# Performance work log

Measured on AMD Instinct MI355X. Metric: run time of the kernel, lower is better.

## Reference

```python
import jax, jax.numpy as jnp
import numpy as np

N, E = 50000, 800000
DIN, DH, DOUT = 128, 128, 64


def setup_inputs() -> dict:
    key = jax.random.key(0)
    ks = jax.random.split(key, 18)
    s = 0.05
    inp = {
        "x": jax.random.normal(ks[0], (N, DIN), dtype=jnp.float32),
        "edge_index": jax.random.randint(ks[1], (2, E), 0, N, dtype=jnp.int64),
        # conv1 MLP: Linear(DIN,DH), Linear(DH,DH)
        "c1_w1": jax.random.normal(ks[2], (DIN, DH), dtype=jnp.float32) * s,
        "c1_b1": jax.random.normal(ks[3], (DH,), dtype=jnp.float32) * s,
        "c1_w2": jax.random.normal(ks[4], (DH, DH), dtype=jnp.float32) * s,
        "c1_b2": jax.random.normal(ks[5], (DH,), dtype=jnp.float32) * s,
        # conv2 MLP
        "c2_w1": jax.random.normal(ks[6], (DH, DH), dtype=jnp.float32) * s,
        "c2_b1": jax.random.normal(ks[7], (DH,), dtype=jnp.float32) * s,
        "c2_w2": jax.random.normal(ks[8], (DH, DH), dtype=jnp.float32) * s,
        "c2_b2": jax.random.normal(ks[9], (DH,), dtype=jnp.float32) * s,
        # conv3 MLP
        "c3_w1": jax.random.normal(ks[10], (DH, DH), dtype=jnp.float32) * s,
        "c3_b1": jax.random.normal(ks[11], (DH,), dtype=jnp.float32) * s,
        "c3_w2": jax.random.normal(ks[12], (DH, DH), dtype=jnp.float32) * s,
        "c3_b2": jax.random.normal(ks[13], (DH,), dtype=jnp.float32) * s,
        # output head
        "lin1_w": jax.random.normal(ks[14], (DH, DH), dtype=jnp.float32) * s,
        "lin1_b": jax.random.normal(ks[15], (DH,), dtype=jnp.float32) * s,
        "lin2_w": jax.random.normal(ks[16], (DH, DOUT), dtype=jnp.float32) * s,
        "lin2_b": jax.random.normal(ks[17], (DOUT,), dtype=jnp.float32) * s,
    }
    return inp


def _gin_conv(h, src, dst, w1, b1, w2, b2):
    # PyG GINConv, eps=0: MLP((1+eps)*x + sum_{j->i} x_j)
    agg = jax.ops.segment_sum(h[src], dst, num_segments=h.shape[0])  # [N, D]
    z = h + agg
    z = jax.nn.relu(z @ w1 + b1)
    return jax.nn.relu(z @ w2 + b2)


def reference(x, edge_index, c1_w1, c1_b1, c1_w2, c1_b2,
              c2_w1, c2_b1, c2_w2, c2_b2,
              c3_w1, c3_b1, c3_w2, c3_b2,
              lin1_w, lin1_b, lin2_w, lin2_b):
    src, dst = edge_index[0], edge_index[1]
    h = _gin_conv(x, src, dst, c1_w1, c1_b1, c1_w2, c1_b2)
    h = jax.nn.relu(h)  # redundant after MLP ReLU, but faithful to source
    h = _gin_conv(h, src, dst, c2_w1, c2_b1, c2_w2, c2_b2)
    h = jax.nn.relu(h)
    h = _gin_conv(h, src, dst, c3_w1, c3_b1, c3_w2, c3_b2)
    h = jax.nn.relu(h @ lin1_w + lin1_b)
    return h @ lin2_w + lin2_b  # [N, DOUT]
```

## Files before the change

kernel.cpp:

```cpp
#include <hip/hip_runtime.h>
#include <hip/hip_bf16.h>

typedef __attribute__((ext_vector_type(8))) short bf16x8;
typedef __attribute__((ext_vector_type(4))) float f32x4;

#define DH 128
#define DOUT 64

static __device__ __forceinline__ unsigned short f2bf(float f) {
    __hip_bfloat16 h = __float2bfloat16(f);
    return *(unsigned short*)&h;
}
static __device__ __forceinline__ void acc2(float& a0, float& a1, unsigned int u) {
    a0 += __uint_as_float(u << 16);
    a1 += __uint_as_float(u & 0xffff0000u);
}


struct WPrep {
    const float* src[8];
    unsigned short* dst[8];
};

__global__ void prep_kernel(const float* __restrict__ x, unsigned short* __restrict__ xb,
                            unsigned short* __restrict__ hA, unsigned short* __restrict__ hB,
                            int n4, WPrep p, int* __restrict__ cnt,
                            int* __restrict__ esrc, int Epad, int N_) {
    int id = blockIdx.x * blockDim.x + threadIdx.x;
    if (id < n4) {
        float4 v = ((const float4*)x)[id];
        ushort4 b;
        b.x = f2bf(v.x); b.y = f2bf(v.y); b.z = f2bf(v.z); b.w = f2bf(v.w);
        ((ushort4*)xb)[id] = b;
        return;
    }
    id -= n4;
    if (id < N_) { cnt[id] = 0; return; }
    id -= N_;
    if (id < 7 * 16384 + 8192) {
        int m, off;
        if (id < 7 * 16384) { m = id >> 14; off = id & 16383; }
        else { m = 7; off = id - 7 * 16384; }
        int shift = (m == 7) ? 6 : 7;
        int nc = 1 << shift;
        int k = off >> shift;
        int n = off & (nc - 1);
        p.dst[m][n * 128 + k] = f2bf(p.src[m][off]);
        return;
    }
    id -= 7 * 16384 + 8192;
    if (id < 3 * 128) {
        int j = id & 127, w = id >> 7;
        if (w == 0) xb[(size_t)N_ * 128 + j] = 0;
        else if (w == 1) hA[(size_t)N_ * 128 + j] = 0;
        else hB[(size_t)N_ * 128 + j] = 0;
        return;
    }
    id -= 384;
    if (id < Epad) esrc[id] = N_ << 8;
}


__global__ void hist_kernel(const int* __restrict__ dst, int* __restrict__ cnt,
                            int* __restrict__ rank, int E, int n) {
    int e = blockIdx.x * blockDim.x + threadIdx.x;
    if (e < E) {
        int d = dst[e];
        if ((unsigned)d < (unsigned)n) rank[e] = atomicAdd(&cnt[d], 1);
    }
}

__global__ void scan1_kernel(const int* __restrict__ cnt, int* __restrict__ rp_part,
                             int* __restrict__ bsum, int n) {
    __shared__ int s[256];
    int tid = threadIdx.x;
    int i = blockIdx.x * 256 + tid;
    int v = (i < n) ? ((cnt[i] + 7) & ~7) : 0;
    s[tid] = v;
    __syncthreads();
    for (int off = 1; off < 256; off <<= 1) {
        int t = (tid >= off) ? s[tid - off] : 0;
        __syncthreads();
        s[tid] += t;
        __syncthreads();
    }
    if (i <= n) rp_part[i] = s[tid] - v;
    if (tid == 255) bsum[blockIdx.x] = s[255];
}

__global__ void scan2_kernel(int* __restrict__ bsum, int nb) {
    __shared__ int s[256];
    int tid = threadIdx.x;
    int v = (tid < nb) ? bsum[tid] : 0;
    s[tid] = v;
    __syncthreads();
    for (int off = 1; off < 256; off <<= 1) {
        int t = (tid >= off) ? s[tid - off] : 0;
        __syncthreads();
        s[tid] += t;
        __syncthreads();
    }
    if (tid < nb) bsum[tid] = s[tid] - v;
}

__global__ void scan3_fill_kernel(const int* __restrict__ rp_part, const int* __restrict__ bsum,
                                  int* __restrict__ row_ptr,
                                  const int* __restrict__ src, const int* __restrict__ dst,
                                  const int* __restrict__ rank, int* __restrict__ esrc,
                                  int n, int E) {
    int gid = blockIdx.x * blockDim.x + threadIdx.x;
    if (gid <= n) row_ptr[gid] = rp_part[gid] + bsum[gid >> 8];
    if (gid < E) {
        int d = dst[gid];
        if ((unsigned)d < (unsigned)n)
            esrc[rp_part[d] + bsum[d >> 8] + rank[gid]] = src[gid] << 8;
    }
}


template <bool HEAD>
__launch_bounds__(256, 6)
__global__ void layer_kernel(const unsigned short* __restrict__ h,
                             const int* __restrict__ rp,
                             const int* __restrict__ esrc,
                             const unsigned short* __restrict__ W1t,
                             const float* __restrict__ b1,
                             const unsigned short* __restrict__ W2t,
                             const float* __restrict__ b2,
                             const unsigned short* __restrict__ W3t,
                             const float* __restrict__ b3,
                             const unsigned short* __restrict__ W4t,
                             const float* __restrict__ b4,
                             void* __restrict__ outp, int M) {
    constexpr int LDA = 128 + 8;
    constexpr int CAP = 2048;
    __shared__ __align__(16) unsigned short As[16][LDA];
    __shared__ __align__(16) unsigned short Zs[16][LDA];
    __shared__ int sIdx[CAP];

    int tid = threadIdx.x;
    int wave = __builtin_amdgcn_readfirstlane(tid >> 6);
    int lane = tid & 63;
    int row0 = blockIdx.x * 16;
    int nd0 = row0 + wave * 4;

    const char* hc = (const char*)h;
    unsigned voff = (unsigned)lane << 2;

    int wb = rp[row0];
    int C = rp[min(row0 + 16, M)] - wb;

    int b[4], e[4];
    unsigned su[4];
    float a0[4] = {0.f, 0.f, 0.f, 0.f}, a1[4] = {0.f, 0.f, 0.f, 0.f};
#pragma unroll
    for (int i = 0; i < 4; ++i) {
        int nd = nd0 + i;
        int ndc = min(nd, M);
        int nd1 = min(nd + 1, M);
        b[i] = rp[ndc] - wb;
        e[i] = rp[nd1] - wb;
        su[i] = *(const unsigned*)(hc + ((size_t)(unsigned)ndc << 8) + voff);
    }

    for (int p0 = 0; p0 < C; p0 += CAP) {
        int cend = min(C, p0 + CAP);
        for (int i = tid; i < cend - p0; i += 256) sIdx[i] = esrc[wb + p0 + i];
        __syncthreads();
#pragma unroll
        for (int i = 0; i < 4; ++i) {
            int nb = max(b[i], p0) - p0;
            int ne = min(e[i], cend) - p0;
            if (nb < ne) {
                int idxA[8];
                unsigned uA[8];
#pragma unroll
                for (int t = 0; t < 8; ++t) idxA[t] = sIdx[nb + t];
#pragma unroll
                for (int t = 0; t < 8; ++t)
                    uA[t] = *(const unsigned*)(hc + (unsigned)idxA[t] + voff);
                for (int r = nb + 8; r < ne; r += 8) {
                    int idxB[8];
                    unsigned uB[8];
#pragma unroll
                    for (int t = 0; t < 8; ++t) idxB[t] = sIdx[r + t];
#pragma unroll
                    for (int t = 0; t < 8; ++t)
                        uB[t] = *(const unsigned*)(hc + (unsigned)idxB[t] + voff);
#pragma unroll
                    for (int t = 0; t < 8; ++t) acc2(a0[i], a1[i], uA[t]);
#pragma unroll
                    for (int t = 0; t < 8; ++t) { uA[t] = uB[t]; }
                }
#pragma unroll
                for (int t = 0; t < 8; ++t) acc2(a0[i], a1[i], uA[t]);
            }
        }
        __syncthreads();
    }

#pragma unroll
    for (int i = 0; i < 4; ++i) {
        acc2(a0[i], a1[i], su[i]);
        unsigned pv = (unsigned)f2bf(a0[i]) | ((unsigned)f2bf(a1[i]) << 16);
        *(unsigned*)&As[wave * 4 + i][lane * 2] = pv;
    }
    __syncthreads();

    int quad = lane >> 4;
    int l16 = lane & 15;

    bf16x8 af[4];
#pragma unroll
    for (int kt = 0; kt < 4; ++kt)
        af[kt] = *(const bf16x8*)(&As[l16][kt * 32 + quad * 8]);
#pragma unroll
    for (int p = 0; p < 2; ++p) {
        int ncol = (wave * 2 + p) * 16 + l16;
        const unsigned short* wp = W1t + ncol * 128 + quad * 8;
        f32x4 a = {0.f, 0.f, 0.f, 0.f};
#pragma unroll
        for (int kt = 0; kt < 4; ++kt)
            a = __builtin_amdgcn_mfma_f32_16x16x32_bf16(
                af[kt], *(const bf16x8*)(wp + kt * 32), a, 0, 0, 0);
        float bs = b1[ncol];
#pragma unroll
        for (int r = 0; r < 4; ++r) {
            float v = a[r] + bs;
            if (v < 0.f) v = 0.f;
            Zs[quad * 4 + r][ncol] = f2bf(v);
        }
    }
    __syncthreads();

    bf16x8 zf[4];
#pragma unroll
    for (int kt = 0; kt < 4; ++kt)
        zf[kt] = *(const bf16x8*)(&Zs[l16][kt * 32 + quad * 8]);
#pragma unroll
    for (int p = 0; p < 2; ++p) {
        int ncol = (wave * 2 + p) * 16 + l16;
        const unsigned short* wp = W2t + ncol * 128 + quad * 8;
        f32x4 a = {0.f, 0.f, 0.f, 0.f};
#pragma unroll
        for (int kt = 0; kt < 4; ++kt)
            a = __builtin_amdgcn_mfma_f32_16x16x32_bf16(
                zf[kt], *(const bf16x8*)(wp + kt * 32), a, 0, 0, 0);
        float bs = b2[ncol];
#pragma unroll
        for (int r = 0; r < 4; ++r) {
            float v = a[r] + bs;
            if (v < 0.f) v = 0.f;
            if (HEAD) {
                As[quad * 4 + r][ncol] = f2bf(v);
            } else {
                int grow = row0 + quad * 4 + r;
                if (grow < M)
                    ((unsigned short*)outp)[(size_t)grow * 128 + ncol] = f2bf(v);
            }
        }
    }

    if (HEAD) {
        __syncthreads();
        bf16x8 hf[4];
#pragma unroll
        for (int kt = 0; kt < 4; ++kt)
            hf[kt] = *(const bf16x8*)(&As[l16][kt * 32 + quad * 8]);
#pragma unroll
        for (int p = 0; p < 2; ++p) {
            int ncol = (wave * 2 + p) * 16 + l16;
            const unsigned short* wp = W3t + ncol * 128 + quad * 8;
            f32x4 a = {0.f, 0.f, 0.f, 0.f};
#pragma unroll
            for (int kt = 0; kt < 4; ++kt)
                a = __builtin_amdgcn_mfma_f32_16x16x32_bf16(
                    hf[kt], *(const bf16x8*)(wp + kt * 32), a, 0, 0, 0);
            float bs = b3[ncol];
#pragma unroll
            for (int r = 0; r < 4; ++r) {
                float v = a[r] + bs;
                if (v < 0.f) v = 0.f;
                Zs[quad * 4 + r][ncol] = f2bf(v);
            }
        }
        __syncthreads();
        bf16x8 gf[4];
#pragma unroll
        for (int kt = 0; kt < 4; ++kt)
            gf[kt] = *(const bf16x8*)(&Zs[l16][kt * 32 + quad * 8]);
        {
            int ncol = wave * 16 + l16;
            const unsigned short* wp = W4t + ncol * 128 + quad * 8;
            f32x4 a = {0.f, 0.f, 0.f, 0.f};
#pragma unroll
            for (int kt = 0; kt < 4; ++kt)
                a = __builtin_amdgcn_mfma_f32_16x16x32_bf16(
                    gf[kt], *(const bf16x8*)(wp + kt * 32), a, 0, 0, 0);
            float bs = b4[ncol];
#pragma unroll
            for (int r = 0; r < 4; ++r) {
                int grow = row0 + quad * 4 + r;
                if (grow < M)
                    ((float*)outp)[(size_t)grow * 64 + ncol] = a[r] + bs;
            }
        }
    }
}


extern "C" void kernel_launch(void* const* d_in, const int* in_sizes, int n_in,
                              void* d_out, int out_size, void* d_ws, size_t ws_size,
                              hipStream_t stream) {
    const float* x = (const float*)d_in[0];
    const int* ei = (const int*)d_in[1];
    int N = in_sizes[0] / DH;
    int E = in_sizes[1] / 2;
    const int* src = ei;
    const int* dstv = ei + E;
    int Epad = E + 7 * N + 1024;

    char* ws = (char*)d_ws;
    size_t off = 0;
    auto alloc = [&](size_t bytes) -> void* {
        void* p = ws + off;
        off += (bytes + 255) & ~(size_t)255;
        return p;
    };
    unsigned short* xb = (unsigned short*)alloc((size_t)(N + 1) * DH * 2);
    unsigned short* hA = (unsigned short*)alloc((size_t)(N + 1) * DH * 2);
    unsigned short* hB = (unsigned short*)alloc((size_t)(N + 1) * DH * 2);
    unsigned short* wt[8];
    for (int m = 0; m < 8; ++m) wt[m] = (unsigned short*)alloc(16384 * 2);
    int* cnt     = (int*)alloc((size_t)N * 4);
    int* rp_part = (int*)alloc((size_t)(N + 1) * 4);
    int* row_ptr = (int*)alloc((size_t)(N + 1) * 4);
    int* rank    = (int*)alloc((size_t)E * 4);
    int* bsum    = (int*)alloc(256 * 4);
    int* esrc    = (int*)alloc((size_t)Epad * 4);

    WPrep wp;
    wp.src[0] = (const float*)d_in[2];
    wp.src[1] = (const float*)d_in[4];
    wp.src[2] = (const float*)d_in[6];
    wp.src[3] = (const float*)d_in[8];
    wp.src[4] = (const float*)d_in[10];
    wp.src[5] = (const float*)d_in[12];
    wp.src[6] = (const float*)d_in[14];
    wp.src[7] = (const float*)d_in[16];
    for (int m = 0; m < 8; ++m) wp.dst[m] = wt[m];
    int n4 = N * DH / 4;
    int prep_items = n4 + N + 7 * 16384 + 8192 + 384 + Epad;
    prep_kernel<<<(prep_items + 255) / 256, 256, 0, stream>>>(
        x, xb, hA, hB, n4, wp, cnt, esrc, Epad, N);

    int nb = (N + 1 + 255) / 256;
    int eb = (E + 255) / 256;
    hist_kernel<<<eb, 256, 0, stream>>>(dstv, cnt, rank, E, N);
    scan1_kernel<<<nb, 256, 0, stream>>>(cnt, rp_part, bsum, N);
    scan2_kernel<<<1, 256, 0, stream>>>(bsum, nb);
    scan3_fill_kernel<<<eb, 256, 0, stream>>>(rp_part, bsum, row_ptr,
                                              src, dstv, rank, esrc, N, E);

    int gb = (N + 15) / 16;

    const float* c1b1 = (const float*)d_in[3];
    const float* c1b2 = (const float*)d_in[5];
    const float* c2b1 = (const float*)d_in[7];
    const float* c2b2 = (const float*)d_in[9];
    const float* c3b1 = (const float*)d_in[11];
    const float* c3b2 = (const float*)d_in[13];
    const float* l1b  = (const float*)d_in[15];
    const float* l2b  = (const float*)d_in[17];

    layer_kernel<false><<<gb, 256, 0, stream>>>(
        xb, row_ptr, esrc, wt[0], c1b1, wt[1], c1b2,
        nullptr, nullptr, nullptr, nullptr, hA, N);
    layer_kernel<false><<<gb, 256, 0, stream>>>(
        hA, row_ptr, esrc, wt[2], c2b1, wt[3], c2b2,
        nullptr, nullptr, nullptr, nullptr, hB, N);
    layer_kernel<true><<<gb, 256, 0, stream>>>(
        hB, row_ptr, esrc, wt[4], c3b1, wt[5], c3b2,
        wt[6], l1b, wt[7], l2b, d_out, N);
}
```

Before: 322.1 us.

## Pipeline gather across a wave's four nodes and fold histogram into prep

The per-node gather loops become one continuous stream over the wave's contiguous edge range. Four 8-wide load buffers stay in flight, and each batch is routed to the right node accumulator using scalar segment boundaries. The histogram kernel is merged into the prep kernel, cnt is zeroed with a memset, and esrc padding is written only for each node's tail slots instead of over the whole array. Occupancy is raised to 7 waves per SIMD, and the self-feature load moves after the gather. This trades register pressure and branchy accumulation for deeper memory-level parallelism and fewer launches.

```diff
diff --git a/kernel.cpp b/kernel.cpp
--- a/kernel.cpp
+++ b/kernel.cpp
@@ -24,8 +24,9 @@
 
 __global__ void prep_kernel(const float* __restrict__ x, unsigned short* __restrict__ xb,
                             unsigned short* __restrict__ hA, unsigned short* __restrict__ hB,
-                            int n4, WPrep p, int* __restrict__ cnt,
-                            int* __restrict__ esrc, int Epad, int N_) {
+                            int n4, WPrep p,
+                            int* __restrict__ cnt, int* __restrict__ rank,
+                            const int* __restrict__ dstv, int E, int N_) {
     int id = blockIdx.x * blockDim.x + threadIdx.x;
     if (id < n4) {
         float4 v = ((const float4*)x)[id];
@@ -35,8 +36,6 @@
         return;
     }
     id -= n4;
-    if (id < N_) { cnt[id] = 0; return; }
-    id -= N_;
     if (id < 7 * 16384 + 8192) {
         int m, off;
         if (id < 7 * 16384) { m = id >> 14; off = id & 16383; }
@@ -57,18 +56,12 @@
         return;
     }
     id -= 384;
-    if (id < Epad) esrc[id] = N_ << 8;
-}
-
-
-__global__ void hist_kernel(const int* __restrict__ dst, int* __restrict__ cnt,
-                            int* __restrict__ rank, int E, int n) {
-    int e = blockIdx.x * blockDim.x + threadIdx.x;
-    if (e < E) {
-        int d = dst[e];
-        if ((unsigned)d < (unsigned)n) rank[e] = atomicAdd(&cnt[d], 1);
-    }
-}
+    if (id < E) {
+        int d = dstv[id];
+        if ((unsigned)d < (unsigned)N_) rank[id] = atomicAdd(&cnt[d], 1);
+    }
+}
+
 
 __global__ void scan1_kernel(const int* __restrict__ cnt, int* __restrict__ rp_part,
                              int* __restrict__ bsum, int n) {
@@ -106,10 +99,18 @@
 __global__ void scan3_fill_kernel(const int* __restrict__ rp_part, const int* __restrict__ bsum,
                                   int* __restrict__ row_ptr,
                                   const int* __restrict__ src, const int* __restrict__ dst,
-                                  const int* __restrict__ rank, int* __restrict__ esrc,
+                                  const int* __restrict__ rank, const int* __restrict__ cnt,
+                                  int* __restrict__ esrc,
                                   int n, int E) {
     int gid = blockIdx.x * blockDim.x + threadIdx.x;
     if (gid <= n) row_ptr[gid] = rp_part[gid] + bsum[gid >> 8];
+    if (gid < n) {
+        int st = rp_part[gid] + bsum[gid >> 8];
+        int c = cnt[gid];
+        int pe = (c + 7) & ~7;
+        int zr = n << 8;
+        for (int j = c; j < pe; ++j) esrc[st + j] = zr;
+    }
     if (gid < E) {
         int d = dst[gid];
         if ((unsigned)d < (unsigned)n)
@@ -118,8 +119,32 @@
 }
 
 
+#define ACC8(i, U) \
+    _Pragma("unroll") for (int z = 0; z < 8; ++z) acc2(a0[i], a1[i], U[z]);
+
+#define LOAD8(U) \
+    if (q < t) { \
+        int _o = q - p0; \
+        _Pragma("unroll") for (int z = 0; z < 8; ++z) { \
+            unsigned _ix = (unsigned)sIdx[_o + z]; \
+            U[z] = *(const unsigned*)(hc + _ix + voff); \
+        } \
+        q += 8; \
+    }
+
+#define STEP(U) \
+    if (r < t) { \
+        int nn = (r >= sE0 ? 1 : 0) + (r >= sE1 ? 1 : 0) + (r >= sE2 ? 1 : 0); \
+        if (nn == 0) { ACC8(0, U) } \
+        else if (nn == 1) { ACC8(1, U) } \
+        else if (nn == 2) { ACC8(2, U) } \
+        else { ACC8(3, U) } \
+        r += 8; \
+        LOAD8(U) \
+    }
+
 template <bool HEAD>
-__launch_bounds__(256, 6)
+__launch_bounds__(256, 7)
 __global__ void layer_kernel(const unsigned short* __restrict__ h,
                              const int* __restrict__ rp,
                              const int* __restrict__ esrc,
@@ -147,53 +172,35 @@
     const char* hc = (const char*)h;
     unsigned voff = (unsigned)lane << 2;
 
-    int wb = rp[row0];
-    int C = rp[min(row0 + 16, M)] - wb;
-
-    int b[4], e[4];
-    unsigned su[4];
+    int wbv = rp[row0];
+    int Cv = rp[min(row0 + 16, M)] - wbv;
+    int wb = __builtin_amdgcn_readfirstlane(wbv);
+    int C = __builtin_amdgcn_readfirstlane(Cv);
+
+    int bv[5];
+#pragma unroll
+    for (int i = 0; i < 5; ++i) bv[i] = rp[min(nd0 + i, M)] - wb;
+    int sB  = __builtin_amdgcn_readfirstlane(bv[0]);
+    int sE0 = __builtin_amdgcn_readfirstlane(bv[1]);
+    int sE1 = __builtin_amdgcn_readfirstlane(bv[2]);
+    int sE2 = __builtin_amdgcn_readfirstlane(bv[3]);
+    int sE3 = __builtin_amdgcn_readfirstlane(bv[4]);
+
     float a0[4] = {0.f, 0.f, 0.f, 0.f}, a1[4] = {0.f, 0.f, 0.f, 0.f};
-#pragma unroll
-    for (int i = 0; i < 4; ++i) {
-        int nd = nd0 + i;
-        int ndc = min(nd, M);
-        int nd1 = min(nd + 1, M);
-        b[i] = rp[ndc] - wb;
-        e[i] = rp[nd1] - wb;
-        su[i] = *(const unsigned*)(hc + ((size_t)(unsigned)ndc << 8) + voff);
-    }
 
     for (int p0 = 0; p0 < C; p0 += CAP) {
         int cend = min(C, p0 + CAP);
         for (int i = tid; i < cend - p0; i += 256) sIdx[i] = esrc[wb + p0 + i];
         __syncthreads();
-#pragma unroll
-        for (int i = 0; i < 4; ++i) {
-            int nb = max(b[i], p0) - p0;
-            int ne = min(e[i], cend) - p0;
-            if (nb < ne) {
-                int idxA[8];
-                unsigned uA[8];
-#pragma unroll
-                for (int t = 0; t < 8; ++t) idxA[t] = sIdx[nb + t];
-#pragma unroll
-                for (int t = 0; t < 8; ++t)
-                    uA[t] = *(const unsigned*)(hc + (unsigned)idxA[t] + voff);
-                for (int r = nb + 8; r < ne; r += 8) {
-                    int idxB[8];
-                    unsigned uB[8];
-#pragma unroll
-                    for (int t = 0; t < 8; ++t) idxB[t] = sIdx[r + t];
-#pragma unroll
-                    for (int t = 0; t < 8; ++t)
-                        uB[t] = *(const unsigned*)(hc + (unsigned)idxB[t] + voff);
-#pragma unroll
-                    for (int t = 0; t < 8; ++t) acc2(a0[i], a1[i], uA[t]);
-#pragma unroll
-                    for (int t = 0; t < 8; ++t) { uA[t] = uB[t]; }
-                }
-#pragma unroll
-                for (int t = 0; t < 8; ++t) acc2(a0[i], a1[i], uA[t]);
+        int s = max(sB, p0);
+        int t = min(sE3, cend);
+        if (s < t) {
+            unsigned u0[8], u1[8], u2[8], u3[8];
+            int q = s;
+            LOAD8(u0) LOAD8(u1) LOAD8(u2) LOAD8(u3)
+            int r = s;
+            while (r < t) {
+                STEP(u0) STEP(u1) STEP(u2) STEP(u3)
             }
         }
         __syncthreads();
@@ -201,7 +208,9 @@
 
 #pragma unroll
     for (int i = 0; i < 4; ++i) {
-        acc2(a0[i], a1[i], su[i]);
+        int ndc = min(nd0 + i, M);
+        unsigned su = *(const unsigned*)(hc + ((size_t)(unsigned)ndc << 8) + voff);
+        acc2(a0[i], a1[i], su);
         unsigned pv = (unsigned)f2bf(a0[i]) | ((unsigned)f2bf(a1[i]) << 16);
         *(unsigned*)&As[wave * 4 + i][lane * 2] = pv;
     }
@@ -349,18 +358,20 @@
     wp.src[6] = (const float*)d_in[14];
     wp.src[7] = (const float*)d_in[16];
     for (int m = 0; m < 8; ++m) wp.dst[m] = wt[m];
+
+    hipMemsetAsync(cnt, 0, (size_t)N * 4, stream);
+
     int n4 = N * DH / 4;
-    int prep_items = n4 + N + 7 * 16384 + 8192 + 384 + Epad;
+    int prep_items = n4 + 7 * 16384 + 8192 + 384 + E;
     prep_kernel<<<(prep_items + 255) / 256, 256, 0, stream>>>(
-        x, xb, hA, hB, n4, wp, cnt, esrc, Epad, N);
+        x, xb, hA, hB, n4, wp, cnt, rank, dstv, E, N);
 
     int nb = (N + 1 + 255) / 256;
     int eb = (E + 255) / 256;
-    hist_kernel<<<eb, 256, 0, stream>>>(dstv, cnt, rank, E, N);
     scan1_kernel<<<nb, 256, 0, stream>>>(cnt, rp_part, bsum, N);
     scan2_kernel<<<1, 256, 0, stream>>>(bsum, nb);
     scan3_fill_kernel<<<eb, 256, 0, stream>>>(rp_part, bsum, row_ptr,
-                                              src, dstv, rank, esrc, N, E);
+                                              src, dstv, rank, cnt, esrc, N, E);
 
     int gb = (N + 15) / 16;
 
```

New measurement: 323.1 us. No clear change (+0.3%).

## Quantize node features to int8 with per-row scales for gather aggregation

Applied to the files above, without the earlier changes.

Node feature buffers are stored as int8 with one float scale per row instead of bf16, halving the bytes read by the neighbor gather that dominates each GIN layer. The scale of each neighbor is fetched once while staging edge indices into shared memory and is used during accumulation. Layer outputs are written through a shared-memory staging step that computes row maxima and requantizes. Padding-entry fill moves from the prep kernel into the scan/fill kernel, and cnt is zeroed with a memset. This costs accuracy, since 8-bit per-row quantization loses precision relative to bf16 and may break the tolerance check.

```diff
diff --git a/kernel.cpp b/kernel.cpp
--- a/kernel.cpp
+++ b/kernel.cpp
@@ -11,9 +11,11 @@
     __hip_bfloat16 h = __float2bfloat16(f);
     return *(unsigned short*)&h;
 }
-static __device__ __forceinline__ void acc2(float& a0, float& a1, unsigned int u) {
-    a0 += __uint_as_float(u << 16);
-    a1 += __uint_as_float(u & 0xffff0000u);
+static __device__ __forceinline__ void accI(float& a0, float& a1, unsigned u, float s) {
+    int lo = (int)(signed char)(u & 0xffu);
+    int hi = (int)(signed char)(u >> 8);
+    a0 += s * (float)lo;
+    a1 += s * (float)hi;
 }
 
 
@@ -22,21 +24,28 @@
     unsigned short* dst[8];
 };
 
-__global__ void prep_kernel(const float* __restrict__ x, unsigned short* __restrict__ xb,
-                            unsigned short* __restrict__ hA, unsigned short* __restrict__ hB,
-                            int n4, WPrep p, int* __restrict__ cnt,
-                            int* __restrict__ esrc, int Epad, int N_) {
+__global__ void prep_conv_kernel(const float* __restrict__ x,
+                                 char* __restrict__ xq, float* __restrict__ sx,
+                                 char* __restrict__ hAq, float* __restrict__ sA,
+                                 char* __restrict__ hBq, float* __restrict__ sB,
+                                 int nA, WPrep p, int N_) {
     int id = blockIdx.x * blockDim.x + threadIdx.x;
-    if (id < n4) {
+    if (id < nA) {
         float4 v = ((const float4*)x)[id];
-        ushort4 b;
-        b.x = f2bf(v.x); b.y = f2bf(v.y); b.z = f2bf(v.z); b.w = f2bf(v.w);
-        ((ushort4*)xb)[id] = b;
+        float m = fmaxf(fmaxf(fabsf(v.x), fabsf(v.y)), fmaxf(fabsf(v.z), fabsf(v.w)));
+#pragma unroll
+        for (int d = 16; d >= 1; d >>= 1) m = fmaxf(m, __shfl_xor(m, d));
+        float inv = m > 0.f ? 127.f / m : 0.f;
+        int q0 = __float2int_rn(v.x * inv);
+        int q1 = __float2int_rn(v.y * inv);
+        int q2 = __float2int_rn(v.z * inv);
+        int q3 = __float2int_rn(v.w * inv);
+        unsigned pk = (q0 & 0xff) | ((q1 & 0xff) << 8) | ((q2 & 0xff) << 16) | ((q3 & 0xff) << 24);
+        ((unsigned*)xq)[id] = pk;
+        if ((id & 31) == 0) sx[id >> 5] = m * (1.f / 127.f);
         return;
     }
-    id -= n4;
-    if (id < N_) { cnt[id] = 0; return; }
-    id -= N_;
+    id -= nA;
     if (id < 7 * 16384 + 8192) {
         int m, off;
         if (id < 7 * 16384) { m = id >> 14; off = id & 16383; }
@@ -49,26 +58,28 @@
         return;
     }
     id -= 7 * 16384 + 8192;
-    if (id < 3 * 128) {
-        int j = id & 127, w = id >> 7;
-        if (w == 0) xb[(size_t)N_ * 128 + j] = 0;
-        else if (w == 1) hA[(size_t)N_ * 128 + j] = 0;
-        else hB[(size_t)N_ * 128 + j] = 0;
+    if (id < 96) {
+        int w = id >> 5, j = id & 31;
+        unsigned* dst = (unsigned*)(w == 0 ? xq : (w == 1 ? hAq : hBq));
+        dst[(size_t)N_ * 32 + j] = 0u;
         return;
     }
-    id -= 384;
-    if (id < Epad) esrc[id] = N_ << 8;
-}
-
-
-__global__ void hist_kernel(const int* __restrict__ dst, int* __restrict__ cnt,
-                            int* __restrict__ rank, int E, int n) {
+    id -= 96;
+    if (id < 3) {
+        (id == 0 ? sx : (id == 1 ? sA : sB))[N_] = 0.f;
+    }
+}
+
+
+__global__ void prep_hist_kernel(const int* __restrict__ dstv, int* __restrict__ cnt,
+                                 int* __restrict__ rank, int E, int N_) {
     int e = blockIdx.x * blockDim.x + threadIdx.x;
     if (e < E) {
-        int d = dst[e];
-        if ((unsigned)d < (unsigned)n) rank[e] = atomicAdd(&cnt[d], 1);
-    }
-}
+        int d = dstv[e];
+        if ((unsigned)d < (unsigned)N_) rank[e] = atomicAdd(&cnt[d], 1);
+    }
+}
+
 
 __global__ void scan1_kernel(const int* __restrict__ cnt, int* __restrict__ rp_part,
                              int* __restrict__ bsum, int n) {
@@ -106,21 +117,29 @@
 __global__ void scan3_fill_kernel(const int* __restrict__ rp_part, const int* __restrict__ bsum,
                                   int* __restrict__ row_ptr,
                                   const int* __restrict__ src, const int* __restrict__ dst,
-                                  const int* __restrict__ rank, int* __restrict__ esrc,
+                                  const int* __restrict__ rank, const int* __restrict__ cnt,
+                                  int* __restrict__ esrc,
                                   int n, int E) {
     int gid = blockIdx.x * blockDim.x + threadIdx.x;
     if (gid <= n) row_ptr[gid] = rp_part[gid] + bsum[gid >> 8];
+    if (gid < n) {
+        int st = rp_part[gid] + bsum[gid >> 8];
+        int c = cnt[gid];
+        int pe = (c + 7) & ~7;
+        int zr = n << 7;
+        for (int j = c; j < pe; ++j) esrc[st + j] = zr;
+    }
     if (gid < E) {
         int d = dst[gid];
         if ((unsigned)d < (unsigned)n)
-            esrc[rp_part[d] + bsum[d >> 8] + rank[gid]] = src[gid] << 8;
+            esrc[rp_part[d] + bsum[d >> 8] + rank[gid]] = src[gid] << 7;
     }
 }
 
 
 template <bool HEAD>
 __launch_bounds__(256, 6)
-__global__ void layer_kernel(const unsigned short* __restrict__ h,
+__global__ void layer_kernel(const char* __restrict__ hq, const float* __restrict__ sIn,
                              const int* __restrict__ rp,
                              const int* __restrict__ esrc,
                              const unsigned short* __restrict__ W1t,
@@ -131,12 +150,13 @@
                              const float* __restrict__ b3,
                              const unsigned short* __restrict__ W4t,
                              const float* __restrict__ b4,
-                             void* __restrict__ outp, int M) {
+                             char* __restrict__ outq, float* __restrict__ outs,
+                             float* __restrict__ outp, int M) {
     constexpr int LDA = 128 + 8;
-    constexpr int CAP = 2048;
+    constexpr int CAP = 1024;
     __shared__ __align__(16) unsigned short As[16][LDA];
     __shared__ __align__(16) unsigned short Zs[16][LDA];
-    __shared__ int sIdx[CAP];
+    __shared__ __align__(16) int2 sIdx[CAP];
 
     int tid = threadIdx.x;
     int wave = __builtin_amdgcn_readfirstlane(tid >> 6);
@@ -144,56 +164,59 @@
     int row0 = blockIdx.x * 16;
     int nd0 = row0 + wave * 4;
 
-    const char* hc = (const char*)h;
-    unsigned voff = (unsigned)lane << 2;
-
-    int wb = rp[row0];
-    int C = rp[min(row0 + 16, M)] - wb;
+    const char* hc = hq;
+    unsigned voff = (unsigned)lane << 1;
+
+    int wbv = rp[row0];
+    int Cv = rp[min(row0 + 16, M)] - wbv;
+    int wb = __builtin_amdgcn_readfirstlane(wbv);
+    int C = __builtin_amdgcn_readfirstlane(Cv);
 
     int b[4], e[4];
-    unsigned su[4];
-    float a0[4] = {0.f, 0.f, 0.f, 0.f}, a1[4] = {0.f, 0.f, 0.f, 0.f};
 #pragma unroll
     for (int i = 0; i < 4; ++i) {
-        int nd = nd0 + i;
-        int ndc = min(nd, M);
-        int nd1 = min(nd + 1, M);
+        int ndc = min(nd0 + i, M);
+        int nd1 = min(nd0 + i + 1, M);
         b[i] = rp[ndc] - wb;
         e[i] = rp[nd1] - wb;
-        su[i] = *(const unsigned*)(hc + ((size_t)(unsigned)ndc << 8) + voff);
-    }
+    }
+
+    float a0[4] = {0.f, 0.f, 0.f, 0.f}, a1[4] = {0.f, 0.f, 0.f, 0.f};
 
     for (int p0 = 0; p0 < C; p0 += CAP) {
         int cend = min(C, p0 + CAP);
-        for (int i = tid; i < cend - p0; i += 256) sIdx[i] = esrc[wb + p0 + i];
+        for (int i = tid; i < cend - p0; i += 256) {
+            int off = esrc[wb + p0 + i];
+            sIdx[i] = make_int2(off, __float_as_int(sIn[(unsigned)off >> 7]));
+        }
         __syncthreads();
 #pragma unroll
         for (int i = 0; i < 4; ++i) {
             int nb = max(b[i], p0) - p0;
             int ne = min(e[i], cend) - p0;
             if (nb < ne) {
-                int idxA[8];
-                unsigned uA[8];
-#pragma unroll
-                for (int t = 0; t < 8; ++t) idxA[t] = sIdx[nb + t];
+                int2 ia[8];
+                unsigned ua[8];
+#pragma unroll
+                for (int t = 0; t < 8; ++t) ia[t] = sIdx[nb + t];
 #pragma unroll
                 for (int t = 0; t < 8; ++t)
-                    uA[t] = *(const unsigned*)(hc + (unsigned)idxA[t] + voff);
+                    ua[t] = *(const unsigned short*)(hc + (unsigned)ia[t].x + voff);
                 for (int r = nb + 8; r < ne; r += 8) {
-                    int idxB[8];
-                    unsigned uB[8];
-#pragma unroll
-                    for (int t = 0; t < 8; ++t) idxB[t] = sIdx[r + t];
+                    int2 ib[8];
+                    unsigned ub[8];
+#pragma unroll
+                    for (int t = 0; t < 8; ++t) ib[t] = sIdx[r + t];
 #pragma unroll
                     for (int t = 0; t < 8; ++t)
-                        uB[t] = *(const unsigned*)(hc + (unsigned)idxB[t] + voff);
-#pragma unroll
-                    for (int t = 0; t < 8; ++t) acc2(a0[i], a1[i], uA[t]);
-#pragma unroll
-                    for (int t = 0; t < 8; ++t) { uA[t] = uB[t]; }
+                        ub[t] = *(const unsigned short*)(hc + (unsigned)ib[t].x + voff);
+#pragma unroll
+                    for (int t = 0; t < 8; ++t) accI(a0[i], a1[i], ua[t], __int_as_float(ia[t].y));
+#pragma unroll
+                    for (int t = 0; t < 8; ++t) { ia[t] = ib[t]; ua[t] = ub[t]; }
                 }
 #pragma unroll
-                for (int t = 0; t < 8; ++t) acc2(a0[i], a1[i], uA[t]);
+                for (int t = 0; t < 8; ++t) accI(a0[i], a1[i], ua[t], __int_as_float(ia[t].y));
             }
         }
         __syncthreads();
@@ -201,7 +224,9 @@
 
 #pragma unroll
     for (int i = 0; i < 4; ++i) {
-        acc2(a0[i], a1[i], su[i]);
+        int ndc = min(nd0 + i, M);
+        unsigned su = *(const unsigned short*)(hc + ((size_t)(unsigned)ndc << 7) + voff);
+        accI(a0[i], a1[i], su, sIn[ndc]);
         unsigned pv = (unsigned)f2bf(a0[i]) | ((unsigned)f2bf(a1[i]) << 16);
         *(unsigned*)&As[wave * 4 + i][lane * 2] = pv;
     }
@@ -237,31 +262,68 @@
 #pragma unroll
     for (int kt = 0; kt < 4; ++kt)
         zf[kt] = *(const bf16x8*)(&Zs[l16][kt * 32 + quad * 8]);
-#pragma unroll
-    for (int p = 0; p < 2; ++p) {
-        int ncol = (wave * 2 + p) * 16 + l16;
-        const unsigned short* wp = W2t + ncol * 128 + quad * 8;
-        f32x4 a = {0.f, 0.f, 0.f, 0.f};
-#pragma unroll
-        for (int kt = 0; kt < 4; ++kt)
-            a = __builtin_amdgcn_mfma_f32_16x16x32_bf16(
-                zf[kt], *(const bf16x8*)(wp + kt * 32), a, 0, 0, 0);
-        float bs = b2[ncol];
-#pragma unroll
-        for (int r = 0; r < 4; ++r) {
-            float v = a[r] + bs;
-            if (v < 0.f) v = 0.f;
-            if (HEAD) {
+
+    if (!HEAD) {
+        __shared__ float Fs[16][132];
+#pragma unroll
+        for (int p = 0; p < 2; ++p) {
+            int ncol = (wave * 2 + p) * 16 + l16;
+            const unsigned short* wp = W2t + ncol * 128 + quad * 8;
+            f32x4 a = {0.f, 0.f, 0.f, 0.f};
+#pragma unroll
+            for (int kt = 0; kt < 4; ++kt)
+                a = __builtin_amdgcn_mfma_f32_16x16x32_bf16(
+                    zf[kt], *(const bf16x8*)(wp + kt * 32), a, 0, 0, 0);
+            float bs = b2[ncol];
+#pragma unroll
+            for (int r = 0; r < 4; ++r) {
+                float v = a[r] + bs;
+                if (v < 0.f) v = 0.f;
+                Fs[quad * 4 + r][ncol] = v;
+            }
+        }
+        __syncthreads();
+        {
+            int row = tid >> 4;
+            int c0 = (tid & 15) * 8;
+            float v8[8];
+            float m = 0.f;
+#pragma unroll
+            for (int j = 0; j < 8; ++j) { v8[j] = Fs[row][c0 + j]; m = fmaxf(m, v8[j]); }
+#pragma unroll
+            for (int d = 8; d >= 1; d >>= 1) m = fmaxf(m, __shfl_xor(m, d));
+            float inv = m > 0.f ? 127.f / m : 0.f;
+            unsigned w0 = 0, w1 = 0;
+#pragma unroll
+            for (int j = 0; j < 4; ++j) {
+                w0 |= (unsigned)(__float2int_rn(v8[j] * inv) & 0xff) << (8 * j);
+                w1 |= (unsigned)(__float2int_rn(v8[4 + j] * inv) & 0xff) << (8 * j);
+            }
+            int grow = row0 + row;
+            if (grow < M) {
+                uint2 pk = make_uint2(w0, w1);
+                ((uint2*)(outq + (size_t)grow * 128))[tid & 15] = pk;
+                if ((tid & 15) == 0) outs[grow] = m * (1.f / 127.f);
+            }
+        }
+    } else {
+#pragma unroll
+        for (int p = 0; p < 2; ++p) {
+            int ncol = (wave * 2 + p) * 16 + l16;
+            const unsigned short* wp = W2t + ncol * 128 + quad * 8;
+            f32x4 a = {0.f, 0.f, 0.f, 0.f};
+#pragma unroll
+            for (int kt = 0; kt < 4; ++kt)
+                a = __builtin_amdgcn_mfma_f32_16x16x32_bf16(
+                    zf[kt], *(const bf16x8*)(wp + kt * 32), a, 0, 0, 0);
+            float bs = b2[ncol];
+#pragma unroll
+            for (int r = 0; r < 4; ++r) {
+                float v = a[r] + bs;
+                if (v < 0.f) v = 0.f;
                 As[quad * 4 + r][ncol] = f2bf(v);
-            } else {
-                int grow = row0 + quad * 4 + r;
-                if (grow < M)
-                    ((unsigned short*)outp)[(size_t)grow * 128 + ncol] = f2bf(v);
-            }
-        }
-    }
-
-    if (HEAD) {
+            }
+        }
         __syncthreads();
         bf16x8 hf[4];
 #pragma unroll
@@ -302,7 +364,7 @@
             for (int r = 0; r < 4; ++r) {
                 int grow = row0 + quad * 4 + r;
                 if (grow < M)
-                    ((float*)outp)[(size_t)grow * 64 + ncol] = a[r] + bs;
+                    outp[(size_t)grow * 64 + ncol] = a[r] + bs;
             }
         }
     }
@@ -327,9 +389,12 @@
         off += (bytes + 255) & ~(size_t)255;
         return p;
     };
-    unsigned short* xb = (unsigned short*)alloc((size_t)(N + 1) * DH * 2);
-    unsigned short* hA = (unsigned short*)alloc((size_t)(N + 1) * DH * 2);
-    unsigned short* hB = (unsigned short*)alloc((size_t)(N + 1) * DH * 2);
+    char* xq  = (char*)alloc((size_t)(N + 1) * 128);
+    char* hAq = (char*)alloc((size_t)(N + 1) * 128);
+    char* hBq = (char*)alloc((size_t)(N + 1) * 128);
+    float* sx = (float*)alloc((size_t)(N + 1) * 4);
+    float* sA = (float*)alloc((size_t)(N + 1) * 4);
+    float* sB = (float*)alloc((size_t)(N + 1) * 4);
     unsigned short* wt[8];
     for (int m = 0; m < 8; ++m) wt[m] = (unsigned short*)alloc(16384 * 2);
     int* cnt     = (int*)alloc((size_t)N * 4);
@@ -349,18 +414,21 @@
     wp.src[6] = (const float*)d_in[14];
     wp.src[7] = (const float*)d_in[16];
     for (int m = 0; m < 8; ++m) wp.dst[m] = wt[m];
-    int n4 = N * DH / 4;
-    int prep_items = n4 + N + 7 * 16384 + 8192 + 384 + Epad;
-    prep_kernel<<<(prep_items + 255) / 256, 256, 0, stream>>>(
-        x, xb, hA, hB, n4, wp, cnt, esrc, Epad, N);
+
+    hipMemsetAsync(cnt, 0, (size_t)N * 4, stream);
+
+    int nA = N * 32;
+    int conv_items = nA + 7 * 16384 + 8192 + 99;
+    prep_conv_kernel<<<(conv_items + 255) / 256, 256, 0, stream>>>(
+        x, xq, sx, hAq, sA, hBq, sB, nA, wp, N);
+    prep_hist_kernel<<<(E + 255) / 256, 256, 0, stream>>>(dstv, cnt, rank, E, N);
 
     int nb = (N + 1 + 255) / 256;
     int eb = (E + 255) / 256;
-    hist_kernel<<<eb, 256, 0, stream>>>(dstv, cnt, rank, E, N);
     scan1_kernel<<<nb, 256, 0, stream>>>(cnt, rp_part, bsum, N);
     scan2_kernel<<<1, 256, 0, stream>>>(bsum, nb);
     scan3_fill_kernel<<<eb, 256, 0, stream>>>(rp_part, bsum, row_ptr,
-                                              src, dstv, rank, esrc, N, E);
+                                              src, dstv, rank, cnt, esrc, N, E);
 
     int gb = (N + 15) / 16;
 
@@ -374,12 +442,12 @@
     const float* l2b  = (const float*)d_in[17];
 
     layer_kernel<false><<<gb, 256, 0, stream>>>(
-        xb, row_ptr, esrc, wt[0], c1b1, wt[1], c1b2,
-        nullptr, nullptr, nullptr, nullptr, hA, N);
+        xq, sx, row_ptr, esrc, wt[0], c1b1, wt[1], c1b2,
+        nullptr, nullptr, nullptr, nullptr, hAq, sA, nullptr, N);
     layer_kernel<false><<<gb, 256, 0, stream>>>(
-        hA, row_ptr, esrc, wt[2], c2b1, wt[3], c2b2,
-        nullptr, nullptr, nullptr, nullptr, hB, N);
+        hAq, sA, row_ptr, esrc, wt[2], c2b1, wt[3], c2b2,
+        nullptr, nullptr, nullptr, nullptr, hBq, sB, nullptr, N);
     layer_kernel<true><<<gb, 256, 0, stream>>>(
-        hB, row_ptr, esrc, wt[4], c3b1, wt[5], c3b2,
-        wt[6], l1b, wt[7], l2b, d_out, N);
-}
+        hBq, sB, row_ptr, esrc, wt[4], c3b1, wt[5], c3b2,
+        wt[6], l1b, wt[7], l2b, nullptr, nullptr, (float*)d_out, N);
+}
```

Result: no change. 319.7 us (-0.8%).
